# Performance work log

Hardware: AMD Instinct MI355X
Metric: run time of the kernel (lower is better)

## Reference

```python
import jax, jax.numpy as jnp
import numpy as np

EPS = 1e-8

def _rms(x, g):
    return x / jnp.sqrt(jnp.mean(x * x, axis=-1, keepdims=True) + EPS) * g

def _rope_cos_sin(seq, dim, dtype):
    # base 10000 hardcoded in the original (_init_rope_rop_emb), rope_theta unused
    inv = 1.0 / (10000.0 ** (jnp.arange(0, dim, 2, dtype=jnp.float32) / dim))
    ang = jnp.arange(seq, dtype=jnp.float32)[:, None] * inv[None, :]   # [S, D/2]
    ang = jnp.repeat(ang, 2, axis=-1)                                   # [S, D] pairwise-equal
    return jnp.cos(ang).astype(dtype)[None, None], jnp.sin(ang).astype(dtype)[None, None]

def _rotate(x):
    # interleaved pairs (x0, x1) -> (-x1, x0), matches trans() in apply_rope
    B, H, S, D = x.shape
    xp = x.reshape(B, H, S, D // 2, 2)
    return jnp.stack((-xp[..., 1], xp[..., 0]), axis=-1).reshape(B, H, S, D)

def setup_inputs() -> dict:
    key = jax.random.key(0)
    ks = jax.random.split(key, 16)
    B, S, Hd = 4, 1024, 2048
    nH, nKV = 16, 4
    I = Hd  # intermediate_size must equal hidden_dim for the original FFN to shape-check
    s = 0.02
    inp = {
        'encoder_input': jax.random.normal(ks[0], (B, S, Hd), dtype=jnp.float32),
        'seq_mask': jnp.ones((B, S, 1), dtype=jnp.float32),
        'num_heads': 16,
        'num_kv_heads': 4,
        'g_in': jnp.ones((Hd,), dtype=jnp.float32),
        'g_ffn': jnp.ones((Hd,), dtype=jnp.float32),
        'w_q': jax.random.normal(ks[1], (Hd, Hd), dtype=jnp.float32) * s,
        'b_q': jnp.zeros((Hd,), dtype=jnp.float32),
        'w_k': jax.random.normal(ks[2], (Hd, nKV * (Hd // nH)), dtype=jnp.float32) * s,
        'b_k': jnp.zeros((nKV * (Hd // nH),), dtype=jnp.float32),
        'w_v': jax.random.normal(ks[3], (Hd, nKV * (Hd // nH)), dtype=jnp.float32) * s,
        'b_v': jnp.zeros((nKV * (Hd // nH),), dtype=jnp.float32),
        'w_o': jax.random.normal(ks[4], (Hd, Hd), dtype=jnp.float32) * s,
        'b_o': jnp.zeros((Hd,), dtype=jnp.float32),
        'w_gate': jax.random.normal(ks[5], (Hd, I), dtype=jnp.float32) * s,
        'b_gate': jnp.zeros((I,), dtype=jnp.float32),
        'w_up': jax.random.normal(ks[6], (I, Hd), dtype=jnp.float32) * s,
        'b_up': jnp.zeros((Hd,), dtype=jnp.float32),
        'w_down': jax.random.normal(ks[7], (Hd, I), dtype=jnp.float32) * s,
        'b_down': jnp.zeros((I,), dtype=jnp.float32),
    }
    return inp

def reference(encoder_input, seq_mask, num_heads, num_kv_heads, g_in, g_ffn,
              w_q, b_q, w_k, b_k, w_v, b_v, w_o, b_o,
              w_gate, b_gate, w_up, b_up, w_down, b_down):
    B, S, Hd = encoder_input.shape
    D = Hd // num_heads
    grp = num_heads // num_kv_heads

    x = _rms(encoder_input, g_in)
    q = (x @ w_q + b_q).reshape(B, S, num_heads, D).transpose(0, 2, 1, 3)      # [B,H,S,D]
    k = (x @ w_k + b_k).reshape(B, S, num_kv_heads, D).transpose(0, 2, 1, 3)   # [B,Kh,S,D]
    v = (x @ w_v + b_v).reshape(B, S, num_kv_heads, D).transpose(0, 2, 1, 3)

    cos, sin = _rope_cos_sin(S, D, x.dtype)
    q = cos * q + sin * _rotate(q)
    k = cos * k + sin * _rotate(k)

    # GQA: expand kv heads (unsqueeze/expand/reshape == grouped repeat)
    k = jnp.repeat(k, grp, axis=1)
    v = jnp.repeat(v, grp, axis=1)

    scores = jnp.einsum('bhsd,bhtd->bhst', q, k) / (float(D) ** 0.5)
    mask = jnp.einsum('bsi,bti->bst', seq_mask, seq_mask)[:, None]             # [B,1,S,S]
    scores = jnp.where(mask == 0, -1e30, scores)
    attn = jax.nn.softmax(scores, axis=-1)
    ctx = jnp.einsum('bhst,bhtd->bshd', attn, v).reshape(B, S, Hd)
    attn_out = encoder_input + (ctx @ w_o + b_o)

    h = _rms(attn_out, g_ffn)
    gate = h @ w_gate + b_gate
    up = h @ w_up + b_up
    gate = gate * jax.nn.sigmoid(gate)      # SiLU
    ffn = (up * gate) @ w_down + b_down
    return attn_out + ffn
```

## Files before the change

### kernel.cpp

```cpp
#include <hip/hip_runtime.h>
#include <cstdint>
#include <cstddef>

typedef __bf16 bf16;
typedef __bf16 bf16x4 __attribute__((ext_vector_type(4)));
typedef __bf16 bf16x8 __attribute__((ext_vector_type(8)));
typedef float  f32x4  __attribute__((ext_vector_type(4)));

#define GLD_LDS16(gp, lp)                                                     \
  __builtin_amdgcn_global_load_lds(                                           \
      (__attribute__((address_space(1))) void*)(gp),                          \
      (__attribute__((address_space(3))) void*)(lp), 16, 0, 0)

__device__ __forceinline__ float exp2_hw(float x) {
  float r;
  asm("v_exp_f32 %0, %1" : "=v"(r) : "v"(x));
  return r;
}

__global__ __launch_bounds__(256) void k_transpose(const float* __restrict__ W,
                                                   bf16* __restrict__ Wt,
                                                   int K, int N) {
  __shared__ float tile[64][65];
  int n0 = blockIdx.x * 64, k0 = blockIdx.y * 64;
  int t = threadIdx.x;
  int c4 = (t & 15) * 4, r = t >> 4;
#pragma unroll
  for (int j = 0; j < 4; ++j) {
    f32x4 v = *(const f32x4*)&W[(size_t)(k0 + r + j * 16) * N + n0 + c4];
    tile[r + j * 16][c4 + 0] = v[0];
    tile[r + j * 16][c4 + 1] = v[1];
    tile[r + j * 16][c4 + 2] = v[2];
    tile[r + j * 16][c4 + 3] = v[3];
  }
  __syncthreads();
#pragma unroll
  for (int j = 0; j < 4; ++j) {
    int n = r + j * 16;
    bf16x4 o;
    o[0] = (bf16)tile[c4 + 0][n];
    o[1] = (bf16)tile[c4 + 1][n];
    o[2] = (bf16)tile[c4 + 2][n];
    o[3] = (bf16)tile[c4 + 3][n];
    *(bf16x4*)&Wt[(size_t)(n0 + n) * K + k0 + c4] = o;
  }
}

__global__ __launch_bounds__(256) void k_rmsnorm(const float* __restrict__ X,
                                                 const float* __restrict__ g,
                                                 bf16* __restrict__ Y) {
  int row = blockIdx.x, t = threadIdx.x;
  const float* x = X + (size_t)row * 2048;
  f32x4 v0 = *(const f32x4*)&x[t * 8];
  f32x4 v1 = *(const f32x4*)&x[t * 8 + 4];
  float ss = v0[0] * v0[0] + v0[1] * v0[1] + v0[2] * v0[2] + v0[3] * v0[3] +
             v1[0] * v1[0] + v1[1] * v1[1] + v1[2] * v1[2] + v1[3] * v1[3];
#pragma unroll
  for (int m = 32; m >= 1; m >>= 1) ss += __shfl_xor(ss, m, 64);
  __shared__ float red[4];
  if ((t & 63) == 0) red[t >> 6] = ss;
  __syncthreads();
  ss = red[0] + red[1] + red[2] + red[3];
  float inv = rsqrtf(ss * (1.0f / 2048.0f) + 1e-8f);
  f32x4 g0 = *(const f32x4*)&g[t * 8];
  f32x4 g1 = *(const f32x4*)&g[t * 8 + 4];
  bf16x8 o;
#pragma unroll
  for (int j = 0; j < 4; ++j) {
    o[j]     = (bf16)(v0[j] * inv * g0[j]);
    o[j + 4] = (bf16)(v1[j] * inv * g1[j]);
  }
  *(bf16x8*)&Y[(size_t)row * 2048 + t * 8] = o;
}

__global__ void k_rope_table(float* __restrict__ cosT, float* __restrict__ sinT) {
  int i = blockIdx.x * 256 + threadIdx.x;
  int s = i >> 6, j = i & 63;
  float ang = (float)s * powf(10000.0f, -(float)(2 * j) * (1.0f / 128.0f));
  cosT[i] = cosf(ang);
  sinT[i] = sinf(ang);
}

__global__ __launch_bounds__(256) void k_rope_q(const bf16* __restrict__ qkv,
                                                const float* __restrict__ cosT,
                                                const float* __restrict__ sinT,
                                                bf16* __restrict__ qr) {
  int idx = blockIdx.x * 256 + threadIdx.x;
  int jg = idx & 15, h = (idx >> 4) & 15, bs = idx >> 8;
  int s = bs & 1023, b = bs >> 10;
  bf16x8 v = *(const bf16x8*)&qkv[(size_t)bs * 3072 + h * 128 + jg * 8];
  f32x4 c  = *(const f32x4*)&cosT[(s << 6) + jg * 4];
  f32x4 sn = *(const f32x4*)&sinT[(s << 6) + jg * 4];
  bf16x8 o;
  const float sc = 0.12751743f;
#pragma unroll
  for (int p = 0; p < 4; ++p) {
    float x0 = (float)v[2 * p], x1 = (float)v[2 * p + 1];
    o[2 * p]     = (bf16)((c[p] * x0 - sn[p] * x1) * sc);
    o[2 * p + 1] = (bf16)((c[p] * x1 + sn[p] * x0) * sc);
  }
  *(bf16x8*)&qr[(((size_t)(b * 16 + h)) * 1024 + s) * 128 + jg * 8] = o;
}

__global__ __launch_bounds__(256) void k_rope_k(const bf16* __restrict__ qkv,
                                                const float* __restrict__ cosT,
                                                const float* __restrict__ sinT,
                                                bf16* __restrict__ kr) {
  int idx = blockIdx.x * 256 + threadIdx.x;
  int jg = idx & 15, h = (idx >> 4) & 3, bs = idx >> 6;
  int s = bs & 1023, b = bs >> 10;
  bf16x8 v = *(const bf16x8*)&qkv[(size_t)bs * 3072 + 2048 + h * 128 + jg * 8];
  f32x4 c  = *(const f32x4*)&cosT[(s << 6) + jg * 4];
  f32x4 sn = *(const f32x4*)&sinT[(s << 6) + jg * 4];
  bf16x8 o;
#pragma unroll
  for (int p = 0; p < 4; ++p) {
    float x0 = (float)v[2 * p], x1 = (float)v[2 * p + 1];
    o[2 * p]     = (bf16)(c[p] * x0 - sn[p] * x1);
    o[2 * p + 1] = (bf16)(c[p] * x1 + sn[p] * x0);
  }
  *(bf16x8*)&kr[(((size_t)(b * 4 + h)) * 1024 + s) * 128 + jg * 8] = o;
}

__global__ void k_vtrans(const bf16* __restrict__ qkv, bf16* __restrict__ vt) {
  __shared__ bf16 tile[32][33];
  int s0 = blockIdx.x * 32, d0 = blockIdx.y * 32, bk = blockIdx.z;
  int b = bk >> 2, kh = bk & 3;
  int tx = threadIdx.x, ty = threadIdx.y;
#pragma unroll
  for (int j = 0; j < 32; j += 8)
    tile[ty + j][tx] =
        qkv[((size_t)(b * 1024) + s0 + ty + j) * 3072 + 2560 + kh * 128 + d0 + tx];
  __syncthreads();
#pragma unroll
  for (int j = 0; j < 32; j += 8)
    vt[(((size_t)(b * 4 + kh)) * 128 + d0 + ty + j) * 1024 + s0 + tx] =
        tile[tx][ty + j];
}

#define BAR() __builtin_amdgcn_s_barrier()
#define LGKM0()                                                                \
  {                                                                            \
    asm volatile("s_waitcnt lgkmcnt(0)" ::: "memory");                         \
    __builtin_amdgcn_sched_barrier(0);                                         \
  }
#define LDAQ(MB, AS)                                                           \
  _Pragma("unroll") for (int mi = 0; mi < 4; ++mi)                             \
      _Pragma("unroll") for (int kh = 0; kh < 2; ++kh) {                       \
    int row = wr * 128 + ((MB) + mi) * 16 + lr;                                \
    a[mi * 2 + kh] =                                                           \
        *(const bf16x8*)&(AS)[row * 64 + (((kh * 4 + lq) ^ (lr & 7)) << 3)];   \
  }
#define LDBQ(NB, BS, BF)                                                       \
  _Pragma("unroll") for (int ni = 0; ni < 2; ++ni)                             \
      _Pragma("unroll") for (int kh = 0; kh < 2; ++kh) {                       \
    int row = wc * WTN + ((NB) + ni) * 16 + lr;                                \
    (BF)[ni * 2 + kh] =                                                        \
        *(const bf16x8*)&(BS)[row * 64 + (((kh * 4 + lq) ^ (lr & 7)) << 3)];   \
  }
#define MFQ(MB, NB, BF)                                                        \
  __builtin_amdgcn_s_setprio(1);                                               \
  _Pragma("unroll") for (int mi = 0; mi < 4; ++mi)                             \
      _Pragma("unroll") for (int ni = 0; ni < 2; ++ni)                         \
          _Pragma("unroll") for (int kh = 0; kh < 2; ++kh)                     \
              acc[(MB) + mi][(NB) + ni] =                                      \
      __builtin_amdgcn_mfma_f32_16x16x32_bf16(                                 \
          a[mi * 2 + kh], (BF)[ni * 2 + kh], acc[(MB) + mi][(NB) + ni],        \
          0, 0, 0);                                                            \
  __builtin_amdgcn_s_setprio(0);

template <int BN, int EPI>
__global__ __launch_bounds__(512, 2) void k_gemm8(const bf16* __restrict__ A,
                                                  const bf16* __restrict__ Bt,
                                                  const float* __restrict__ bias,
                                                  const float* __restrict__ res,
                                                  void* __restrict__ Cout,
                                                  int M, int N, int K) {
  (void)M;
  constexpr int WTN = BN / 4;
  constexpr int NR  = WTN / 16;
  constexpr int JA  = 4;
  constexpr int JB  = BN / 64;
  __shared__ alignas(16) bf16 As[2][256 * 64];
  __shared__ alignas(16) bf16 Bs[2][BN * 64];

  int nwg = gridDim.x * gridDim.y;
  int id  = blockIdx.y * gridDim.x + blockIdx.x;
  id = (id & 7) * (nwg >> 3) + (id >> 3);
  int bx = id % gridDim.x, by = id / gridDim.x;
  int m0 = by * 256, n0 = bx * BN;

  int tid = threadIdx.x, w = tid >> 6, lane = tid & 63;
  int lr = lane & 15, lq = lane >> 4;
  int wr = w >> 2, wc = w & 3;
  const bf16* Ag = A  + (size_t)m0 * K;
  const bf16* Bg = Bt + (size_t)n0 * K;

  f32x4 acc[8][NR] = {};
  bf16x8 a[8], bA[4], bB[4];

  auto stage = [&](bf16* dstA, bf16* dstB, int kt) {
#pragma unroll
    for (int j = 0; j < JA; ++j) {
      int s = j * 512 + tid, row = s >> 3, c = (s ^ row) & 7;
      GLD_LDS16(Ag + (size_t)row * K + kt + c * 8, dstA + j * 4096 + w * 512);
    }
#pragma unroll
    for (int j = 0; j < JB; ++j) {
      int s = j * 512 + tid, row = s >> 3, c = (s ^ row) & 7;
      GLD_LDS16(Bg + (size_t)row * K + kt + c * 8, dstB + j * 4096 + w * 512);
    }
  };

  stage(As[0], Bs[0], 0);
  stage(As[1], Bs[1], 64);

  int NP = (K >> 6) >> 1;
  for (int p = 0; p < NP; ++p) {
    bool pf = (p + 1 < NP);
    int kn0 = (2 * p + 2) << 6, kn1 = (2 * p + 3) << 6;

    if constexpr (BN == 256) asm volatile("s_waitcnt vmcnt(8)" ::: "memory");
    else                     asm volatile("s_waitcnt vmcnt(6)" ::: "memory");
    BAR();
    LDAQ(0, As[0]); LDBQ(0, Bs[0], bA);
    BAR(); LGKM0(); MFQ(0, 0, bA); BAR();
    if constexpr (BN == 256) {
      LDBQ(2, Bs[0], bB);
      BAR(); LGKM0(); MFQ(0, 2, bB); BAR();
      LDAQ(4, As[0]);
      BAR(); LGKM0(); MFQ(4, 2, bB); BAR();
      if (pf) stage(As[0], Bs[0], kn0);
      BAR(); MFQ(4, 0, bA); BAR();
    } else {
      LDAQ(4, As[0]);
      BAR(); LGKM0(); MFQ(4, 0, bA); BAR();
      if (pf) stage(As[0], Bs[0], kn0);
    }

    if (pf) {
      if constexpr (BN == 256) asm volatile("s_waitcnt vmcnt(8)" ::: "memory");
      else                     asm volatile("s_waitcnt vmcnt(6)" ::: "memory");
    } else {
      asm volatile("s_waitcnt vmcnt(0)" ::: "memory");
    }
    BAR();

    LDAQ(0, As[1]); LDBQ(0, Bs[1], bA);
    BAR(); LGKM0(); MFQ(0, 0, bA); BAR();
    if constexpr (BN == 256) {
      LDBQ(2, Bs[1], bB);
      BAR(); LGKM0(); MFQ(0, 2, bB); BAR();
      LDAQ(4, As[1]);
      BAR(); LGKM0(); MFQ(4, 2, bB); BAR();
      if (pf) stage(As[1], Bs[1], kn1);
      BAR(); MFQ(4, 0, bA); BAR();
    } else {
      LDAQ(4, As[1]);
      BAR(); LGKM0(); MFQ(4, 0, bA); BAR();
      if (pf) stage(As[1], Bs[1], kn1);
    }
  }

#pragma unroll
  for (int m = 0; m < 8; ++m) {
    int row = m0 + wr * 128 + m * 16 + lq * 4;
#pragma unroll
    for (int n = 0; n < NR; ++n) {
      int col = n0 + wc * WTN + n * 16 + lr;
      float bv = bias[col];
#pragma unroll
      for (int i = 0; i < 4; ++i) {
        float vv = acc[m][n][i] + bv;
        size_t off = (size_t)(row + i) * N + col;
        if constexpr (EPI == 0) ((bf16*)Cout)[off] = (bf16)vv;
        else ((float*)Cout)[off] = vv + res[off];
      }
    }
  }
}

__global__ __launch_bounds__(256) void k_silu_mul(const bf16* __restrict__ gu,
                                                  bf16* __restrict__ prod) {
  int idx = blockIdx.x * 256 + threadIdx.x;
  int r = idx >> 8, cc = (idx & 255) * 8;
  bf16x8 gv = *(const bf16x8*)&gu[(size_t)r * 4096 + cc];
  bf16x8 uv = *(const bf16x8*)&gu[(size_t)r * 4096 + 2048 + cc];
  bf16x8 o;
#pragma unroll
  for (int j = 0; j < 8; ++j) {
    float gf = (float)gv[j], uf = (float)uv[j];
    float sf = gf / (1.0f + __expf(-gf));
    o[j] = (bf16)(uf * sf);
  }
  *(bf16x8*)&prod[(size_t)r * 2048 + cc] = o;
}

__global__ __launch_bounds__(256) void k_flash(const bf16* __restrict__ qr,
                                               const bf16* __restrict__ kr,
                                               const bf16* __restrict__ vt,
                                               bf16* __restrict__ ctx) {
  __shared__ alignas(16) bf16 Ks[2][64][128];
  __shared__ alignas(16) bf16 Vs[2][128][64];
  __shared__ alignas(16) bf16 P[4][16][72];
  int t = threadIdx.x, w = t >> 6, lane = t & 63;
  int lr = lane & 15, lq = lane >> 4;
  int qb = blockIdx.x, bh = blockIdx.y;
  int b = bh >> 4, h = bh & 15, kh = h >> 2;
  const bf16* Q  = qr + ((size_t)bh * 1024 + qb * 64 + w * 16) * 128;
  const bf16* Kp = kr + (size_t)(b * 4 + kh) * 1024 * 128;
  const bf16* Vp = vt + (size_t)(b * 4 + kh) * 128 * 1024;

  bf16x8 aq[4];
#pragma unroll
  for (int kd = 0; kd < 4; ++kd)
    aq[kd] = *(const bf16x8*)&Q[(size_t)lr * 128 + kd * 32 + lq * 8];
  bf16x8 ones;
#pragma unroll
  for (int j = 0; j < 8; ++j) ones[j] = (bf16)1.0f;

  f32x4 accO[8] = {};
  f32x4 accS = {};
  float mrow[4];
#pragma unroll
  for (int i = 0; i < 4; ++i) mrow[i] = -1.0e30f;

  auto stageK = [&](int buf, int kv) {
#pragma unroll
    for (int j = 0; j < 4; ++j) {
      int r = (w * 4 + j) * 4 + (lane >> 4);
      int c = (lane & 15) ^ (r & 7);
      GLD_LDS16(Kp + (size_t)(kv + r) * 128 + c * 8, &Ks[buf][(w * 4 + j) * 4][0]);
    }
  };
  auto stageV = [&](int buf, int kv) {
#pragma unroll
    for (int j = 0; j < 4; ++j) {
      int r = (w * 4 + j) * 8 + (lane >> 3);
      int c = (lane & 7) ^ (r & 7);
      GLD_LDS16(Vp + (size_t)r * 1024 + kv + c * 8, &Vs[buf][(w * 4 + j) * 8][0]);
    }
  };

  stageK(0, 0);
  stageV(0, 0);
  __syncthreads();
  int cur = 0;

  for (int kvt = 0; kvt < 16; ++kvt) {
    if (kvt < 15) { stageK(cur ^ 1, (kvt + 1) * 64); stageV(cur ^ 1, (kvt + 1) * 64); }

    f32x4 sc[4] = {};
    __builtin_amdgcn_s_setprio(1);
#pragma unroll
    for (int n = 0; n < 4; ++n)
#pragma unroll
      for (int kd = 0; kd < 4; ++kd) {
        bf16x8 bk = *(const bf16x8*)&Ks[cur][n * 16 + lr]
                                       [((kd * 4 + lq) ^ (lr & 7)) * 8];
        sc[n] = __builtin_amdgcn_mfma_f32_16x16x32_bf16(aq[kd], bk, sc[n], 0, 0, 0);
      }
    __builtin_amdgcn_s_setprio(0);

    float pl[4];
#pragma unroll
    for (int i = 0; i < 4; ++i)
      pl[i] = fmaxf(fmaxf(sc[0][i], sc[1][i]), fmaxf(sc[2][i], sc[3][i]));
    bool okl = (pl[0] <= mrow[0] + 8.0f) && (pl[1] <= mrow[1] + 8.0f) &&
               (pl[2] <= mrow[2] + 8.0f) && (pl[3] <= mrow[3] + 8.0f);
    if (!__all(okl)) {
#pragma unroll
      for (int i = 0; i < 4; ++i) {
        float v = pl[i];
#pragma unroll
        for (int msk = 8; msk >= 1; msk >>= 1)
          v = fmaxf(v, __shfl_xor(v, msk, 64));
        float mn = fmaxf(mrow[i], v);
        float scl = exp2_hw(mrow[i] - mn);
        mrow[i] = mn;
        accS[i] *= scl;
#pragma unroll
        for (int nc = 0; nc < 8; ++nc) accO[nc][i] *= scl;
      }
    }

#pragma unroll
    for (int n = 0; n < 4; ++n)
#pragma unroll
      for (int i = 0; i < 4; ++i)
        P[w][lq * 4 + i][n * 16 + lr] = (bf16)exp2_hw(sc[n][i] - mrow[i]);

    __builtin_amdgcn_s_setprio(1);
#pragma unroll
    for (int ks = 0; ks < 2; ++ks) {
      bf16x8 pa = *(const bf16x8*)&P[w][lr][ks * 32 + lq * 8];
      accS = __builtin_amdgcn_mfma_f32_16x16x32_bf16(pa, ones, accS, 0, 0, 0);
#pragma unroll
      for (int nc = 0; nc < 8; ++nc) {
        bf16x8 bv = *(const bf16x8*)&Vs[cur][nc * 16 + lr]
                                       [((ks * 4 + lq) ^ (lr & 7)) * 8];
        accO[nc] = __builtin_amdgcn_mfma_f32_16x16x32_bf16(pa, bv, accO[nc], 0, 0, 0);
      }
    }
    __builtin_amdgcn_s_setprio(0);

    __syncthreads();
    cur ^= 1;
  }

#pragma unroll
  for (int i = 0; i < 4; ++i) accS[i] = 1.0f / accS[i];
#pragma unroll
  for (int nc = 0; nc < 8; ++nc)
#pragma unroll
    for (int i = 0; i < 4; ++i) {
      int srow = qb * 64 + w * 16 + lq * 4 + i;
      float ov = accO[nc][i] * accS[i];
      ctx[((size_t)(b * 1024 + srow)) * 2048 + h * 128 + nc * 16 + lr] = (bf16)ov;
    }
}

extern "C" void kernel_launch(void* const* d_in, const int* in_sizes, int n_in,
                              void* d_out, int out_size, void* d_ws, size_t ws_size,
                              hipStream_t stream) {
  (void)in_sizes; (void)n_in; (void)out_size; (void)ws_size;
  const float* enc   = (const float*)d_in[0];
  const float* g_in  = (const float*)d_in[4];
  const float* g_ffn = (const float*)d_in[5];
  const float* w_q   = (const float*)d_in[6];
  const float* b_q   = (const float*)d_in[7];
  const float* w_k   = (const float*)d_in[8];
  const float* b_k   = (const float*)d_in[9];
  const float* w_v   = (const float*)d_in[10];
  const float* b_v   = (const float*)d_in[11];
  const float* w_o   = (const float*)d_in[12];
  const float* b_o   = (const float*)d_in[13];
  const float* w_g   = (const float*)d_in[14];
  const float* b_g   = (const float*)d_in[15];
  const float* w_u   = (const float*)d_in[16];
  const float* b_u   = (const float*)d_in[17];
  const float* w_d   = (const float*)d_in[18];
  const float* b_d   = (const float*)d_in[19];

  char* ws = (char*)d_ws;
  bf16*  wqkv_t = (bf16*)(ws + 0);
  bf16*  wo_t   = (bf16*)(ws + 12582912);
  bf16*  wgu_t  = (bf16*)(ws + 20971520);
  bf16*  wd_t   = (bf16*)(ws + 37748736);
  float* bqkv   = (float*)(ws + 46137344);
  float* bgu    = (float*)(ws + 46149632);
  float* cosT   = (float*)(ws + 46166016);
  float* sinT   = (float*)(ws + 46428160);
  bf16*  xnorm  = (bf16*)(ws + 46690304);
  bf16*  qkvl   = (bf16*)(ws + 63467520);
  bf16*  qrr    = (bf16*)(ws + 88633344);
  bf16*  krr    = (bf16*)(ws + 105410560);
  bf16*  vtt    = (bf16*)(ws + 109604864);
  bf16*  ctx    = (bf16*)(ws + 113799168);
  float* attno  = (float*)(ws + 130576384);

  k_transpose<<<dim3(32, 32), 256, 0, stream>>>(w_q, wqkv_t, 2048, 2048);
  k_transpose<<<dim3( 8, 32), 256, 0, stream>>>(w_k, wqkv_t + (size_t)2048 * 2048, 2048, 512);
  k_transpose<<<dim3( 8, 32), 256, 0, stream>>>(w_v, wqkv_t + (size_t)2560 * 2048, 2048, 512);
  k_transpose<<<dim3(32, 32), 256, 0, stream>>>(w_o, wo_t, 2048, 2048);
  k_transpose<<<dim3(32, 32), 256, 0, stream>>>(w_g, wgu_t, 2048, 2048);
  k_transpose<<<dim3(32, 32), 256, 0, stream>>>(w_u, wgu_t + (size_t)2048 * 2048, 2048, 2048);
  k_transpose<<<dim3(32, 32), 256, 0, stream>>>(w_d, wd_t, 2048, 2048);
  hipMemcpyAsync(bqkv,        b_q, 2048 * 4, hipMemcpyDeviceToDevice, stream);
  hipMemcpyAsync(bqkv + 2048, b_k,  512 * 4, hipMemcpyDeviceToDevice, stream);
  hipMemcpyAsync(bqkv + 2560, b_v,  512 * 4, hipMemcpyDeviceToDevice, stream);
  hipMemcpyAsync(bgu,         b_g, 2048 * 4, hipMemcpyDeviceToDevice, stream);
  hipMemcpyAsync(bgu + 2048,  b_u, 2048 * 4, hipMemcpyDeviceToDevice, stream);
  k_rope_table<<<256, 256, 0, stream>>>(cosT, sinT);

  k_rmsnorm<<<4096, 256, 0, stream>>>(enc, g_in, xnorm);
  k_gemm8<256, 0><<<dim3(12, 16), 512, 0, stream>>>(xnorm, wqkv_t, bqkv, nullptr,
                                                    qkvl, 4096, 3072, 2048);
  k_rope_q<<<4096, 256, 0, stream>>>(qkvl, cosT, sinT, qrr);
  k_rope_k<<<1024, 256, 0, stream>>>(qkvl, cosT, sinT, krr);
  k_vtrans<<<dim3(32, 4, 16), dim3(32, 8), 0, stream>>>(qkvl, vtt);
  k_flash<<<dim3(16, 64), 256, 0, stream>>>(qrr, krr, vtt, ctx);
  k_gemm8<128, 1><<<dim3(16, 16), 512, 0, stream>>>(ctx, wo_t, b_o, enc, attno,
                                                    4096, 2048, 2048);
  k_rmsnorm<<<4096, 256, 0, stream>>>(attno, g_ffn, xnorm);
  k_gemm8<256, 0><<<dim3(16, 16), 512, 0, stream>>>(xnorm, wgu_t, bgu, nullptr,
                                                    qkvl, 4096, 4096, 2048);
  k_silu_mul<<<4096, 256, 0, stream>>>(qkvl, ctx);
  k_gemm8<128, 1><<<dim3(16, 16), 512, 0, stream>>>(ctx, wd_t, b_d, attno,
                                                    (float*)d_out, 4096, 2048, 2048);
}
```

Measured before the change: 541.3 us.

## Fuse SiLU-gate into gate/up GEMM via interleaved weights and simplify GEMM pipeline

Gate and up weight columns and biases are interleaved in 32-column groups so each GEMM tile holds matching gate and up outputs. A new epilogue then computes SiLU(gate)*up directly and writes the bf16 product, which removes the separate silu_mul kernel and the 4096-wide intermediate round trip. The GEMM is also templated on BM and its main loop rewritten from a hand-interleaved two-stage schedule into a simpler per-tile loop. The output-projection and down-projection GEMMs switch to 128x256 tiles. The simpler schedule may lose some of the overlap between LDS loads and MFMA work that the old interleaving provided.

After: 519.0 us. 1.04x faster.

```diff
diff --git a/kernel.cpp b/kernel.cpp
--- a/kernel.cpp
+++ b/kernel.cpp
@@ -18,6 +18,7 @@
   return r;
 }
 
+template <int PERM>
 __global__ __launch_bounds__(256) void k_transpose(const float* __restrict__ W,
                                                    bf16* __restrict__ Wt,
                                                    int K, int N) {
@@ -37,13 +38,25 @@
 #pragma unroll
   for (int j = 0; j < 4; ++j) {
     int n = r + j * 16;
+    int nn = n0 + n, dr;
+    if constexpr (PERM == 0) dr = nn;
+    else if constexpr (PERM == 1) dr = ((nn >> 5) << 6) + (nn & 31);
+    else dr = ((nn >> 5) << 6) + 32 + (nn & 31);
     bf16x4 o;
     o[0] = (bf16)tile[c4 + 0][n];
     o[1] = (bf16)tile[c4 + 1][n];
     o[2] = (bf16)tile[c4 + 2][n];
     o[3] = (bf16)tile[c4 + 3][n];
-    *(bf16x4*)&Wt[(size_t)(n0 + n) * K + k0 + c4] = o;
-  }
+    *(bf16x4*)&Wt[(size_t)dr * K + k0 + c4] = o;
+  }
+}
+
+__global__ void k_bias_il(const float* __restrict__ bg,
+                          const float* __restrict__ bu,
+                          float* __restrict__ il) {
+  int c = blockIdx.x * 256 + threadIdx.x;
+  il[((c >> 5) << 6) + (c & 31)] = bg[c];
+  il[((c >> 5) << 6) + 32 + (c & 31)] = bu[c];
 }
 
 __global__ __launch_bounds__(256) void k_rmsnorm(const float* __restrict__ X,
@@ -138,38 +151,7 @@
         tile[tx][ty + j];
 }
 
-#define BAR() __builtin_amdgcn_s_barrier()
-#define LGKM0()                                                                \
-  {                                                                            \
-    asm volatile("s_waitcnt lgkmcnt(0)" ::: "memory");                         \
-    __builtin_amdgcn_sched_barrier(0);                                         \
-  }
-#define LDAQ(MB, AS)                                                           \
-  _Pragma("unroll") for (int mi = 0; mi < 4; ++mi)                             \
-      _Pragma("unroll") for (int kh = 0; kh < 2; ++kh) {                       \
-    int row = wr * 128 + ((MB) + mi) * 16 + lr;                                \
-    a[mi * 2 + kh] =                                                           \
-        *(const bf16x8*)&(AS)[row * 64 + (((kh * 4 + lq) ^ (lr & 7)) << 3)];   \
-  }
-#define LDBQ(NB, BS, BF)                                                       \
-  _Pragma("unroll") for (int ni = 0; ni < 2; ++ni)                             \
-      _Pragma("unroll") for (int kh = 0; kh < 2; ++kh) {                       \
-    int row = wc * WTN + ((NB) + ni) * 16 + lr;                                \
-    (BF)[ni * 2 + kh] =                                                        \
-        *(const bf16x8*)&(BS)[row * 64 + (((kh * 4 + lq) ^ (lr & 7)) << 3)];   \
-  }
-#define MFQ(MB, NB, BF)                                                        \
-  __builtin_amdgcn_s_setprio(1);                                               \
-  _Pragma("unroll") for (int mi = 0; mi < 4; ++mi)                             \
-      _Pragma("unroll") for (int ni = 0; ni < 2; ++ni)                         \
-          _Pragma("unroll") for (int kh = 0; kh < 2; ++kh)                     \
-              acc[(MB) + mi][(NB) + ni] =                                      \
-      __builtin_amdgcn_mfma_f32_16x16x32_bf16(                                 \
-          a[mi * 2 + kh], (BF)[ni * 2 + kh], acc[(MB) + mi][(NB) + ni],        \
-          0, 0, 0);                                                            \
-  __builtin_amdgcn_s_setprio(0);
-
-template <int BN, int EPI>
+template <int BM, int BN, int EPI>
 __global__ __launch_bounds__(512, 2) void k_gemm8(const bf16* __restrict__ A,
                                                   const bf16* __restrict__ Bt,
                                                   const float* __restrict__ bias,
@@ -177,18 +159,18 @@
                                                   void* __restrict__ Cout,
                                                   int M, int N, int K) {
   (void)M;
-  constexpr int WTN = BN / 4;
-  constexpr int NR  = WTN / 16;
-  constexpr int JA  = 4;
-  constexpr int JB  = BN / 64;
-  __shared__ alignas(16) bf16 As[2][256 * 64];
+  constexpr int WTN = BN / 4, NR = WTN / 16;
+  constexpr int MR  = BM / 32;
+  constexpr int MH  = (MR > 4) ? 4 : MR;
+  constexpr int JA  = BM / 64, JB = BN / 64, LT = JA + JB;
+  __shared__ alignas(16) bf16 As[2][BM * 64];
   __shared__ alignas(16) bf16 Bs[2][BN * 64];
 
   int nwg = gridDim.x * gridDim.y;
   int id  = blockIdx.y * gridDim.x + blockIdx.x;
   id = (id & 7) * (nwg >> 3) + (id >> 3);
   int bx = id % gridDim.x, by = id / gridDim.x;
-  int m0 = by * 256, n0 = bx * BN;
+  int m0 = by * BM, n0 = bx * BN;
 
   int tid = threadIdx.x, w = tid >> 6, lane = tid & 63;
   int lr = lane & 15, lq = lane >> 4;
@@ -196,104 +178,109 @@
   const bf16* Ag = A  + (size_t)m0 * K;
   const bf16* Bg = Bt + (size_t)n0 * K;
 
-  f32x4 acc[8][NR] = {};
-  bf16x8 a[8], bA[4], bB[4];
-
-  auto stage = [&](bf16* dstA, bf16* dstB, int kt) {
+  f32x4 acc[MR][NR] = {};
+  bf16x8 a[MH * 2], b[NR * 2];
+
+  auto stage = [&](int buf, int kt) {
 #pragma unroll
     for (int j = 0; j < JA; ++j) {
       int s = j * 512 + tid, row = s >> 3, c = (s ^ row) & 7;
-      GLD_LDS16(Ag + (size_t)row * K + kt + c * 8, dstA + j * 4096 + w * 512);
+      GLD_LDS16(Ag + (size_t)row * K + kt + c * 8, &As[buf][j * 4096 + w * 512]);
     }
 #pragma unroll
     for (int j = 0; j < JB; ++j) {
       int s = j * 512 + tid, row = s >> 3, c = (s ^ row) & 7;
-      GLD_LDS16(Bg + (size_t)row * K + kt + c * 8, dstB + j * 4096 + w * 512);
+      GLD_LDS16(Bg + (size_t)row * K + kt + c * 8, &Bs[buf][j * 4096 + w * 512]);
     }
   };
 
-  stage(As[0], Bs[0], 0);
-  stage(As[1], Bs[1], 64);
-
-  int NP = (K >> 6) >> 1;
-  for (int p = 0; p < NP; ++p) {
-    bool pf = (p + 1 < NP);
-    int kn0 = (2 * p + 2) << 6, kn1 = (2 * p + 3) << 6;
-
-    if constexpr (BN == 256) asm volatile("s_waitcnt vmcnt(8)" ::: "memory");
-    else                     asm volatile("s_waitcnt vmcnt(6)" ::: "memory");
-    BAR();
-    LDAQ(0, As[0]); LDBQ(0, Bs[0], bA);
-    BAR(); LGKM0(); MFQ(0, 0, bA); BAR();
-    if constexpr (BN == 256) {
-      LDBQ(2, Bs[0], bB);
-      BAR(); LGKM0(); MFQ(0, 2, bB); BAR();
-      LDAQ(4, As[0]);
-      BAR(); LGKM0(); MFQ(4, 2, bB); BAR();
-      if (pf) stage(As[0], Bs[0], kn0);
-      BAR(); MFQ(4, 0, bA); BAR();
-    } else {
-      LDAQ(4, As[0]);
-      BAR(); LGKM0(); MFQ(4, 0, bA); BAR();
-      if (pf) stage(As[0], Bs[0], kn0);
-    }
-
-    if (pf) {
-      if constexpr (BN == 256) asm volatile("s_waitcnt vmcnt(8)" ::: "memory");
-      else                     asm volatile("s_waitcnt vmcnt(6)" ::: "memory");
+  stage(0, 0);
+  stage(1, 64);
+  int NT = K >> 6;
+  for (int t = 0; t < NT; ++t) {
+    if (t + 1 < NT) {
+      if constexpr (LT == 8) asm volatile("s_waitcnt vmcnt(8)" ::: "memory");
+      else                   asm volatile("s_waitcnt vmcnt(6)" ::: "memory");
     } else {
       asm volatile("s_waitcnt vmcnt(0)" ::: "memory");
     }
-    BAR();
-
-    LDAQ(0, As[1]); LDBQ(0, Bs[1], bA);
-    BAR(); LGKM0(); MFQ(0, 0, bA); BAR();
-    if constexpr (BN == 256) {
-      LDBQ(2, Bs[1], bB);
-      BAR(); LGKM0(); MFQ(0, 2, bB); BAR();
-      LDAQ(4, As[1]);
-      BAR(); LGKM0(); MFQ(4, 2, bB); BAR();
-      if (pf) stage(As[1], Bs[1], kn1);
-      BAR(); MFQ(4, 0, bA); BAR();
+    __builtin_amdgcn_s_barrier();
+    const bf16* as = As[t & 1];
+    const bf16* bs = Bs[t & 1];
+    __builtin_amdgcn_s_setprio(1);
+#pragma unroll
+    for (int ni = 0; ni < NR; ++ni)
+#pragma unroll
+      for (int kh = 0; kh < 2; ++kh)
+        b[ni * 2 + kh] = *(const bf16x8*)&bs[(wc * WTN + ni * 16 + lr) * 64 +
+                                             (((kh * 4 + lq) ^ (lr & 7)) << 3)];
+#pragma unroll
+    for (int mi = 0; mi < MH; ++mi)
+#pragma unroll
+      for (int kh = 0; kh < 2; ++kh)
+        a[mi * 2 + kh] = *(const bf16x8*)&as[(wr * (BM / 2) + mi * 16 + lr) * 64 +
+                                             (((kh * 4 + lq) ^ (lr & 7)) << 3)];
+#pragma unroll
+    for (int mi = 0; mi < MH; ++mi)
+#pragma unroll
+      for (int ni = 0; ni < NR; ++ni)
+#pragma unroll
+        for (int kh = 0; kh < 2; ++kh)
+          acc[mi][ni] = __builtin_amdgcn_mfma_f32_16x16x32_bf16(
+              a[mi * 2 + kh], b[ni * 2 + kh], acc[mi][ni], 0, 0, 0);
+    if constexpr (MR == 8) {
+#pragma unroll
+      for (int mi = 0; mi < 4; ++mi)
+#pragma unroll
+        for (int kh = 0; kh < 2; ++kh)
+          a[mi * 2 + kh] = *(const bf16x8*)&as[(wr * (BM / 2) + (4 + mi) * 16 + lr) * 64 +
+                                               (((kh * 4 + lq) ^ (lr & 7)) << 3)];
+#pragma unroll
+      for (int mi = 0; mi < 4; ++mi)
+#pragma unroll
+        for (int ni = 0; ni < NR; ++ni)
+#pragma unroll
+          for (int kh = 0; kh < 2; ++kh)
+            acc[4 + mi][ni] = __builtin_amdgcn_mfma_f32_16x16x32_bf16(
+                a[mi * 2 + kh], b[ni * 2 + kh], acc[4 + mi][ni], 0, 0, 0);
+    }
+    __builtin_amdgcn_s_setprio(0);
+    __builtin_amdgcn_s_barrier();
+    if (t + 2 < NT) stage(t & 1, (t + 2) << 6);
+  }
+
+#pragma unroll
+  for (int m = 0; m < MR; ++m) {
+    int row = m0 + wr * (BM / 2) + m * 16 + lq * 4;
+    if constexpr (EPI == 2) {
+#pragma unroll
+      for (int n = 0; n < 2; ++n) {
+        float bg = bias[n0 + wc * WTN + n * 16 + lr];
+        float bu = bias[n0 + wc * WTN + (n + 2) * 16 + lr];
+        int col = bx * (BN / 2) + wc * (WTN / 2) + n * 16 + lr;
+#pragma unroll
+        for (int i = 0; i < 4; ++i) {
+          float g = acc[m][n][i] + bg;
+          float u = acc[m][n + 2][i] + bu;
+          float sg = g / (1.0f + __expf(-g));
+          ((bf16*)Cout)[(size_t)(row + i) * (N / 2) + col] = (bf16)(u * sg);
+        }
+      }
     } else {
-      LDAQ(4, As[1]);
-      BAR(); LGKM0(); MFQ(4, 0, bA); BAR();
-      if (pf) stage(As[1], Bs[1], kn1);
-    }
-  }
-
-#pragma unroll
-  for (int m = 0; m < 8; ++m) {
-    int row = m0 + wr * 128 + m * 16 + lq * 4;
-#pragma unroll
-    for (int n = 0; n < NR; ++n) {
-      int col = n0 + wc * WTN + n * 16 + lr;
-      float bv = bias[col];
-#pragma unroll
-      for (int i = 0; i < 4; ++i) {
-        float vv = acc[m][n][i] + bv;
-        size_t off = (size_t)(row + i) * N + col;
-        if constexpr (EPI == 0) ((bf16*)Cout)[off] = (bf16)vv;
-        else ((float*)Cout)[off] = vv + res[off];
+#pragma unroll
+      for (int n = 0; n < NR; ++n) {
+        int col = n0 + wc * WTN + n * 16 + lr;
+        float bv = bias[col];
+#pragma unroll
+        for (int i = 0; i < 4; ++i) {
+          float vv = acc[m][n][i] + bv;
+          size_t off = (size_t)(row + i) * N + col;
+          if constexpr (EPI == 0) ((bf16*)Cout)[off] = (bf16)vv;
+          else ((float*)Cout)[off] = vv + res[off];
+        }
       }
     }
   }
-}
-
-__global__ __launch_bounds__(256) void k_silu_mul(const bf16* __restrict__ gu,
-                                                  bf16* __restrict__ prod) {
-  int idx = blockIdx.x * 256 + threadIdx.x;
-  int r = idx >> 8, cc = (idx & 255) * 8;
-  bf16x8 gv = *(const bf16x8*)&gu[(size_t)r * 4096 + cc];
-  bf16x8 uv = *(const bf16x8*)&gu[(size_t)r * 4096 + 2048 + cc];
-  bf16x8 o;
-#pragma unroll
-  for (int j = 0; j < 8; ++j) {
-    float gf = (float)gv[j], uf = (float)uv[j];
-    float sf = gf / (1.0f + __expf(-gf));
-    o[j] = (bf16)(uf * sf);
-  }
-  *(bf16x8*)&prod[(size_t)r * 2048 + cc] = o;
 }
 
 __global__ __launch_bounds__(256) void k_flash(const bf16* __restrict__ qr,
@@ -459,33 +446,31 @@
   bf16*  ctx    = (bf16*)(ws + 113799168);
   float* attno  = (float*)(ws + 130576384);
 
-  k_transpose<<<dim3(32, 32), 256, 0, stream>>>(w_q, wqkv_t, 2048, 2048);
-  k_transpose<<<dim3( 8, 32), 256, 0, stream>>>(w_k, wqkv_t + (size_t)2048 * 2048, 2048, 512);
-  k_transpose<<<dim3( 8, 32), 256, 0, stream>>>(w_v, wqkv_t + (size_t)2560 * 2048, 2048, 512);
-  k_transpose<<<dim3(32, 32), 256, 0, stream>>>(w_o, wo_t, 2048, 2048);
-  k_transpose<<<dim3(32, 32), 256, 0, stream>>>(w_g, wgu_t, 2048, 2048);
-  k_transpose<<<dim3(32, 32), 256, 0, stream>>>(w_u, wgu_t + (size_t)2048 * 2048, 2048, 2048);
-  k_transpose<<<dim3(32, 32), 256, 0, stream>>>(w_d, wd_t, 2048, 2048);
+  k_transpose<0><<<dim3(32, 32), 256, 0, stream>>>(w_q, wqkv_t, 2048, 2048);
+  k_transpose<0><<<dim3( 8, 32), 256, 0, stream>>>(w_k, wqkv_t + (size_t)2048 * 2048, 2048, 512);
+  k_transpose<0><<<dim3( 8, 32), 256, 0, stream>>>(w_v, wqkv_t + (size_t)2560 * 2048, 2048, 512);
+  k_transpose<0><<<dim3(32, 32), 256, 0, stream>>>(w_o, wo_t, 2048, 2048);
+  k_transpose<1><<<dim3(32, 32), 256, 0, stream>>>(w_g, wgu_t, 2048, 2048);
+  k_transpose<2><<<dim3(32, 32), 256, 0, stream>>>(w_u, wgu_t, 2048, 2048);
+  k_transpose<0><<<dim3(32, 32), 256, 0, stream>>>(w_d, wd_t, 2048, 2048);
   hipMemcpyAsync(bqkv,        b_q, 2048 * 4, hipMemcpyDeviceToDevice, stream);
   hipMemcpyAsync(bqkv + 2048, b_k,  512 * 4, hipMemcpyDeviceToDevice, stream);
   hipMemcpyAsync(bqkv + 2560, b_v,  512 * 4, hipMemcpyDeviceToDevice, stream);
-  hipMemcpyAsync(bgu,         b_g, 2048 * 4, hipMemcpyDeviceToDevice, stream);
-  hipMemcpyAsync(bgu + 2048,  b_u, 2048 * 4, hipMemcpyDeviceToDevice, stream);
+  k_bias_il<<<8, 256, 0, stream>>>(b_g, b_u, bgu);
   k_rope_table<<<256, 256, 0, stream>>>(cosT, sinT);
 
   k_rmsnorm<<<4096, 256, 0, stream>>>(enc, g_in, xnorm);
-  k_gemm8<256, 0><<<dim3(12, 16), 512, 0, stream>>>(xnorm, wqkv_t, bqkv, nullptr,
-                                                    qkvl, 4096, 3072, 2048);
+  k_gemm8<256, 256, 0><<<dim3(12, 16), 512, 0, stream>>>(xnorm, wqkv_t, bqkv,
+      nullptr, qkvl, 4096, 3072, 2048);
   k_rope_q<<<4096, 256, 0, stream>>>(qkvl, cosT, sinT, qrr);
   k_rope_k<<<1024, 256, 0, stream>>>(qkvl, cosT, sinT, krr);
   k_vtrans<<<dim3(32, 4, 16), dim3(32, 8), 0, stream>>>(qkvl, vtt);
   k_flash<<<dim3(16, 64), 256, 0, stream>>>(qrr, krr, vtt, ctx);
-  k_gemm8<128, 1><<<dim3(16, 16), 512, 0, stream>>>(ctx, wo_t, b_o, enc, attno,
-                                                    4096, 2048, 2048);
+  k_gemm8<128, 256, 1><<<dim3(8, 32), 512, 0, stream>>>(ctx, wo_t, b_o, enc,
+      attno, 4096, 2048, 2048);
   k_rmsnorm<<<4096, 256, 0, stream>>>(attno, g_ffn, xnorm);
-  k_gemm8<256, 0><<<dim3(16, 16), 512, 0, stream>>>(xnorm, wgu_t, bgu, nullptr,
-                                                    qkvl, 4096, 4096, 2048);
-  k_silu_mul<<<4096, 256, 0, stream>>>(qkvl, ctx);
-  k_gemm8<128, 1><<<dim3(16, 16), 512, 0, stream>>>(ctx, wd_t, b_d, attno,
-                                                    (float*)d_out, 4096, 2048, 2048);
-}
+  k_gemm8<256, 256, 2><<<dim3(16, 16), 512, 0, stream>>>(xnorm, wgu_t, bgu,
+      nullptr, ctx, 4096, 4096, 2048);
+  k_gemm8<128, 256, 1><<<dim3(8, 32), 512, 0, stream>>>(ctx, wd_t, b_d, attno,
+      (float*)d_out, 4096, 2048, 2048);
+}
```
